# Performance work log

Measured on AMD Instinct MI355X. Metric: run time of the kernel, lower is better.

Reference implementation:

```python
import jax, jax.numpy as jnp
import numpy as np

QKV = 1024   # qkv_size (input feature dim)
E = 64       # embed_size (per-head dim)
H = 16       # num_heads
OUT = 1024   # output_size
B, S = 8, 1024


def setup_inputs() -> dict:
    key = jax.random.key(0)
    ks = jax.random.split(key, 8)
    inv = 1.0 / np.sqrt(QKV)
    return {
        "query": jax.random.normal(ks[0], (B, S, QKV), jnp.float32),
        "key": jax.random.normal(ks[1], (B, S, QKV), jnp.float32),
        "value": jax.random.normal(ks[2], (B, S, QKV), jnp.float32),
        # stacked per-head projection weights, torch Linear convention y = x @ W.T -> store as [H, QKV, E]
        "Wq": jax.random.normal(ks[3], (H, QKV, E), jnp.float32) * inv,
        "Wk": jax.random.normal(ks[4], (H, QKV, E), jnp.float32) * inv,
        "Wv": jax.random.normal(ks[5], (H, QKV, E), jnp.float32) * inv,
        "Wo": jax.random.normal(ks[6], (OUT, H * E), jnp.float32) / np.sqrt(H * E),
        "bo": jax.random.normal(ks[7], (OUT,), jnp.float32) * 0.01,
    }


def reference(query, key, value, Wq, Wk, Wv, Wo, bo):
    # batched over heads: [B,S,QKV] x [H,QKV,E] -> [B,H,S,E]
    Q = jnp.einsum("bsd,hde->bhse", query, Wq)
    K = jnp.einsum("bsd,hde->bhse", key, Wk)
    V = jnp.einsum("bsd,hde->bhse", value, Wv)
    # NOTE: original scales by sqrt(qkv_dim) (input dim), not per-head dim
    scale = 1.0 / jnp.sqrt(jnp.float32(QKV))
    scores = jnp.einsum("bhse,bhte->bhst", Q, K) * scale  # [B,H,S,S]
    attn = jax.nn.softmax(scores, axis=-1)
    attended = jnp.einsum("bhst,bhte->bhse", attn, V)     # [B,H,S,E]
    # concat heads along last dim (head-major order matches torch.cat of head outputs)
    concat = attended.transpose(0, 2, 1, 3).reshape(query.shape[0], query.shape[1], H * E)
    return concat @ Wo.T + bo
```

## Files before the change

kernel.cpp:

```cpp
#include <hip/hip_runtime.h>
#include <stdint.h>


typedef __bf16 bf16x8 __attribute__((ext_vector_type(8)));
typedef float f32x4 __attribute__((ext_vector_type(4)));

typedef __attribute__((address_space(3))) uint32_t lds_u32;
typedef const __attribute__((address_space(1))) uint32_t glb_u32;

__device__ __forceinline__ ushort f2bf(float f) {
  uint32_t x = __float_as_uint(f);
  x += 0x7fff + ((x >> 16) & 1);
  return (ushort)(x >> 16);
}
__device__ __forceinline__ bf16x8 ld8(const ushort* p) {
  union { uint4 u; bf16x8 b; } c;
  c.u = *reinterpret_cast<const uint4*>(p);
  return c.b;
}
__device__ __forceinline__ void cvt16(const float* __restrict__ src,
                                      ushort* __restrict__ dst) {
  union { uint4 u[2]; ushort s[16]; } o;
#pragma unroll
  for (int i = 0; i < 4; ++i) {
    const float4 f = reinterpret_cast<const float4*>(src)[i];
    o.s[4 * i + 0] = f2bf(f.x);
    o.s[4 * i + 1] = f2bf(f.y);
    o.s[4 * i + 2] = f2bf(f.z);
    o.s[4 * i + 3] = f2bf(f.w);
  }
  reinterpret_cast<uint4*>(dst)[0] = o.u[0];
  reinterpret_cast<uint4*>(dst)[1] = o.u[1];
}

__device__ __forceinline__ void gld16(const ushort* g, ushort* l) {
  __builtin_amdgcn_global_load_lds((glb_u32*)g, (lds_u32*)l, 16, 0, 0);
}

__global__ __launch_bounds__(256) void prep_wt3(
    const float* __restrict__ W0, const float* __restrict__ W1,
    const float* __restrict__ W2, ushort* __restrict__ T0,
    ushort* __restrict__ T1, ushort* __restrict__ T2) {
  __shared__ __align__(16) ushort tile[64 * 72];
  const int sel = blockIdx.x >> 8;
  const float* W = sel == 0 ? W0 : sel == 1 ? W1 : W2;
  ushort* WT = sel == 0 ? T0 : sel == 1 ? T1 : T2;
  const int bid = blockIdx.x & 255;
  const int h = bid >> 4;
  const int kt = bid & 15;
  const int t = threadIdx.x;
  const int row = t >> 2;
  const int ch = (t & 3) * 16;
  cvt16(W + ((size_t)h * 1024 + kt * 64 + row) * 64 + ch, &tile[row * 72 + ch]);
  __syncthreads();
  const int e = t >> 2;
  const int kc = (t & 3) * 16;
  ushort vals[16];
#pragma unroll
  for (int j = 0; j < 16; ++j) vals[j] = tile[(kc + j) * 72 + e];
  ushort* dst = WT + (size_t)(h * 64 + e) * 1024 + kt * 64 + kc;
  reinterpret_cast<uint4*>(dst)[0] = *reinterpret_cast<uint4*>(&vals[0]);
  reinterpret_cast<uint4*>(dst)[1] = *reinterpret_cast<uint4*>(&vals[8]);
}

__global__ __launch_bounds__(256) void cvt_wo(const float* __restrict__ src,
                                              ushort* __restrict__ dst) {
  const int i = (blockIdx.x * 256 + threadIdx.x) * 16;
  cvt16(src + i, dst + i);
}

__global__ __launch_bounds__(256) void cvt3(const float* __restrict__ s0,
                                            ushort* __restrict__ d0,
                                            const float* __restrict__ s1,
                                            ushort* __restrict__ d1,
                                            const float* __restrict__ s2,
                                            ushort* __restrict__ d2) {
  int b = blockIdx.x;
  const float* s;
  ushort* d;
  if (b < 2048) { s = s0; d = d0; }
  else if (b < 4096) { s = s1; d = d1; b -= 2048; }
  else { s = s2; d = d2; b -= 4096; }
  const int i = (b * 256 + threadIdx.x) * 16;
  cvt16(s + i, d + i);
}

__device__ __forceinline__ void stage_ab(const ushort* a_src,
                                         const ushort* b_src, ushort* as,
                                         ushort* bs, int w, int k0) {
#pragma unroll
  for (int c = 0; c < 4; ++c) {
    gld16(a_src + (size_t)c * 32 * 1024 + k0, as + (w * 8 + c * 32) * 64);
    gld16(b_src + (size_t)c * 32 * 1024 + k0, bs + (w * 8 + c * 32) * 64);
  }
}

template <bool F32OUT>
__device__ __forceinline__ void gemm_core(const ushort* __restrict__ A,
                                          const ushort* __restrict__ Bt,
                                          const float* __restrict__ bias,
                                          void* __restrict__ Cv, float oscale,
                                          int bx, int by) {
  __shared__ __align__(16) ushort As[2][128 * 64];
  __shared__ __align__(16) ushort Bs[2][128 * 64];
  const int n0 = bx * 128;
  const int m0 = by * 128;
  const int t = threadIdx.x;
  const int lane = t & 63;
  const int w = t >> 6;
  const int wm = w >> 1, wn = w & 1;
  const int col = lane & 15;
  const int quad = lane >> 4;
  const int gr = lane >> 3;
  const int gc = (lane & 7) * 8;

  f32x4 acc[4][4];
#pragma unroll
  for (int i = 0; i < 4; ++i)
#pragma unroll
    for (int j = 0; j < 4; ++j) acc[i][j] = (f32x4){0.f, 0.f, 0.f, 0.f};

  const ushort* a_src = A + (size_t)(m0 + w * 8 + gr) * 1024 + gc;
  const ushort* b_src = Bt + (size_t)(n0 + w * 8 + gr) * 1024 + gc;

  stage_ab(a_src, b_src, As[0], Bs[0], w, 0);
  __syncthreads();

  int cur = 0;
  for (int it = 0; it < 16; ++it) {
    if (it < 15)
      stage_ab(a_src, b_src, As[cur ^ 1], Bs[cur ^ 1], w, (it + 1) * 64);
    const ushort* asb = As[cur];
    const ushort* bsb = Bs[cur];
#pragma unroll
    for (int half = 0; half < 2; ++half) {
      bf16x8 af[4], bfr[4];
#pragma unroll
      for (int i = 0; i < 4; ++i)
        af[i] = ld8(&asb[(wm * 64 + i * 16 + col) * 64 + half * 32 + quad * 8]);
#pragma unroll
      for (int j = 0; j < 4; ++j)
        bfr[j] = ld8(&bsb[(wn * 64 + j * 16 + col) * 64 + half * 32 + quad * 8]);
#pragma unroll
      for (int i = 0; i < 4; ++i)
#pragma unroll
        for (int j = 0; j < 4; ++j)
          acc[i][j] = __builtin_amdgcn_mfma_f32_16x16x32_bf16(af[i], bfr[j],
                                                              acc[i][j], 0, 0, 0);
    }
    __syncthreads();
    cur ^= 1;
  }

#pragma unroll
  for (int i = 0; i < 4; ++i)
#pragma unroll
    for (int j = 0; j < 4; ++j) {
      const int n = n0 + wn * 64 + j * 16 + col;
      float bv = 0.f;
      if (F32OUT) bv = bias[n];
#pragma unroll
      for (int r = 0; r < 4; ++r) {
        const int m = m0 + wm * 64 + i * 16 + quad * 4 + r;
        if (F32OUT)
          reinterpret_cast<float*>(Cv)[(size_t)m * 1024 + n] = acc[i][j][r] + bv;
        else
          reinterpret_cast<ushort*>(Cv)[(size_t)m * 1024 + n] =
              f2bf(acc[i][j][r] * oscale);
      }
    }
}

template <bool F32OUT>
__global__ __launch_bounds__(256) void gemm_bb(const ushort* __restrict__ A,
                                               const ushort* __restrict__ Bt,
                                               const float* __restrict__ bias,
                                               void* __restrict__ Cv,
                                               float oscale) {
  gemm_core<F32OUT>(A, Bt, bias, Cv, oscale, blockIdx.x, blockIdx.y);
}

__global__ __launch_bounds__(256) void gemm_proj2(
    const ushort* __restrict__ A0, const ushort* __restrict__ B0,
    ushort* __restrict__ C0, float s0, const ushort* __restrict__ A1,
    const ushort* __restrict__ B1, ushort* __restrict__ C1, float s1) {
  if (blockIdx.z == 0)
    gemm_core<false>(A0, B0, nullptr, C0, s0, blockIdx.x, blockIdx.y);
  else
    gemm_core<false>(A1, B1, nullptr, C1, s1, blockIdx.x, blockIdx.y);
}

__global__ __launch_bounds__(256) void flash_attn(const ushort* __restrict__ Q,
                                                  const ushort* __restrict__ K,
                                                  const ushort* __restrict__ V,
                                                  ushort* __restrict__ O) {
  __shared__ __align__(16) ushort QP[128 * 72];
  __shared__ __align__(16) ushort Ks[64 * 64];
  __shared__ __align__(16) ushort Vt[64 * 72];
  const int pair = blockIdx.x & 127;
  const int b = pair >> 4;
  const int h = pair & 15;
  const int qt = blockIdx.x >> 7;
  const int t = threadIdx.x;
  const int lane = t & 63;
  const int w = t >> 6;
  const int col = lane & 15;
  const int quad = lane >> 4;

  const size_t base = (size_t)b * 1024 * 1024 + h * 64;
  const int qrow0 = qt * 128;

  {
    const int row = t >> 1;
    const int c0 = (t & 1) * 32;
    const ushort* src = Q + base + (size_t)(qrow0 + row) * 1024 + c0;
    uint4 v0 = reinterpret_cast<const uint4*>(src)[0];
    uint4 v1 = reinterpret_cast<const uint4*>(src)[1];
    uint4 v2 = reinterpret_cast<const uint4*>(src)[2];
    uint4 v3 = reinterpret_cast<const uint4*>(src)[3];
    reinterpret_cast<uint4*>(&QP[row * 72 + c0])[0] = v0;
    reinterpret_cast<uint4*>(&QP[row * 72 + c0])[1] = v1;
    reinterpret_cast<uint4*>(&QP[row * 72 + c0])[2] = v2;
    reinterpret_cast<uint4*>(&QP[row * 72 + c0])[3] = v3;
  }
  __syncthreads();
  bf16x8 qa[2][2];
#pragma unroll
  for (int g = 0; g < 2; ++g)
#pragma unroll
    for (int half = 0; half < 2; ++half)
      qa[g][half] =
          ld8(&QP[(w * 32 + g * 16 + col) * 72 + half * 32 + quad * 8]);

  f32x4 o_[2][4];
#pragma unroll
  for (int g = 0; g < 2; ++g)
#pragma unroll
    for (int c = 0; c < 4; ++c) o_[g][c] = (f32x4){0.f, 0.f, 0.f, 0.f};
  float m_s[2] = {-1e30f, -1e30f};
  float l_s[2] = {0.f, 0.f};

  const int krow = w * 16 + (lane >> 3);
  const int kcs = (((lane & 7) ^ (lane >> 3)) << 3);
  const int s7 = col & 7;

  for (int kt = 0; kt < 16; ++kt) {
    {
      const ushort* k0 = K + base + (size_t)(kt * 64 + krow) * 1024 + kcs;
      gld16(k0, &Ks[(w * 16) * 64]);
      gld16(k0 + 8 * 1024, &Ks[(w * 16 + 8) * 64]);
      const int vs = t & 63;
      const int ve = (t >> 6) * 16;
      const ushort* vsrc = V + base + (size_t)(kt * 64 + vs) * 1024 + ve;
      union { uint4 u[2]; ushort s[16]; } vv;
      vv.u[0] = reinterpret_cast<const uint4*>(vsrc)[0];
      vv.u[1] = reinterpret_cast<const uint4*>(vsrc)[1];
#pragma unroll
      for (int j = 0; j < 16; ++j) Vt[(ve + j) * 72 + vs] = vv.s[j];
    }
    __syncthreads();

    f32x4 sc[2][4];
#pragma unroll
    for (int c = 0; c < 4; ++c) {
      const int R = (c * 16 + col) * 64;
      bf16x8 kb0 = ld8(&Ks[R + ((quad ^ s7) << 3)]);
      bf16x8 kb1 = ld8(&Ks[R + (((quad + 4) ^ s7) << 3)]);
#pragma unroll
      for (int g = 0; g < 2; ++g) {
        f32x4 z = {0.f, 0.f, 0.f, 0.f};
        z = __builtin_amdgcn_mfma_f32_16x16x32_bf16(kb0, qa[g][0], z, 0, 0, 0);
        z = __builtin_amdgcn_mfma_f32_16x16x32_bf16(kb1, qa[g][1], z, 0, 0, 0);
        sc[g][c] = z;
      }
    }

    float al[2];
#pragma unroll
    for (int g = 0; g < 2; ++g) {
      float mx = sc[g][0][0];
#pragma unroll
      for (int c = 0; c < 4; ++c)
#pragma unroll
        for (int r = 0; r < 4; ++r) mx = fmaxf(mx, sc[g][c][r]);
      mx = fmaxf(mx, __shfl_xor(mx, 16));
      mx = fmaxf(mx, __shfl_xor(mx, 32));
      const float m_new = fmaxf(m_s[g], mx);
      al[g] = __expf(m_s[g] - m_new);
      m_s[g] = m_new;
      float rs = 0.f;
      const int prow = (w * 32 + g * 16 + col) * 72;
#pragma unroll
      for (int c = 0; c < 4; ++c) {
        const float p0 = __expf(sc[g][c][0] - m_new);
        const float p1 = __expf(sc[g][c][1] - m_new);
        const float p2 = __expf(sc[g][c][2] - m_new);
        const float p3 = __expf(sc[g][c][3] - m_new);
        rs += (p0 + p1) + (p2 + p3);
        union { uint2 u; ushort s[4]; } pk;
        pk.s[0] = f2bf(p0);
        pk.s[1] = f2bf(p1);
        pk.s[2] = f2bf(p2);
        pk.s[3] = f2bf(p3);
        *reinterpret_cast<uint2*>(&QP[prow + c * 16 + quad * 4]) = pk.u;
      }
      rs += __shfl_xor(rs, 16);
      rs += __shfl_xor(rs, 32);
      l_s[g] = l_s[g] * al[g] + rs;
    }

#pragma unroll
    for (int g = 0; g < 2; ++g)
#pragma unroll
      for (int r = 0; r < 4; ++r) {
        const float a = __shfl(al[g], (lane & 48) | (quad * 4 + r));
        o_[g][0][r] *= a;
        o_[g][1][r] *= a;
        o_[g][2][r] *= a;
        o_[g][3][r] *= a;
      }

    bf16x8 pa[2][2];
#pragma unroll
    for (int g = 0; g < 2; ++g)
#pragma unroll
      for (int half = 0; half < 2; ++half)
        pa[g][half] =
            ld8(&QP[(w * 32 + g * 16 + col) * 72 + half * 32 + quad * 8]);
#pragma unroll
    for (int c = 0; c < 4; ++c) {
      bf16x8 vb0 = ld8(&Vt[(c * 16 + col) * 72 + quad * 8]);
      bf16x8 vb1 = ld8(&Vt[(c * 16 + col) * 72 + 32 + quad * 8]);
#pragma unroll
      for (int g = 0; g < 2; ++g) {
        o_[g][c] = __builtin_amdgcn_mfma_f32_16x16x32_bf16(pa[g][0], vb0,
                                                           o_[g][c], 0, 0, 0);
        o_[g][c] = __builtin_amdgcn_mfma_f32_16x16x32_bf16(pa[g][1], vb1,
                                                           o_[g][c], 0, 0, 0);
      }
    }
    __syncthreads();
  }

#pragma unroll
  for (int g = 0; g < 2; ++g)
#pragma unroll
    for (int r = 0; r < 4; ++r) {
      const float lr = __shfl(l_s[g], (lane & 48) | (quad * 4 + r));
      const float inv = 1.f / lr;
      const size_t row =
          base + (size_t)(qrow0 + w * 32 + g * 16 + quad * 4 + r) * 1024;
      O[row + 0 + col] = f2bf(o_[g][0][r] * inv);
      O[row + 16 + col] = f2bf(o_[g][1][r] * inv);
      O[row + 32 + col] = f2bf(o_[g][2][r] * inv);
      O[row + 48 + col] = f2bf(o_[g][3][r] * inv);
    }
}

extern "C" void kernel_launch(void* const* d_in, const int* in_sizes, int n_in,
                              void* d_out, int out_size, void* d_ws, size_t ws_size,
                              hipStream_t stream) {
  const float* q = (const float*)d_in[0];
  const float* k = (const float*)d_in[1];
  const float* v = (const float*)d_in[2];
  const float* Wq = (const float*)d_in[3];
  const float* Wk = (const float*)d_in[4];
  const float* Wv = (const float*)d_in[5];
  const float* Wo = (const float*)d_in[6];
  const float* bo = (const float*)d_in[7];
  float* out = (float*)d_out;
  ushort* ws = (ushort*)d_ws;

  const size_t M8 = 8u << 20;
  const size_t M1 = 1u << 20;
  ushort* Qp = ws;
  ushort* Kp = ws + M8;
  ushort* Vp = ws + 2 * M8;
  ushort* WqT = ws + 3 * M8;
  ushort* WkT = WqT + M1;
  ushort* WvT = WkT + M1;
  ushort* WoB = WvT + M1;

  ushort* X0 = (ushort*)d_out;
  ushort* X1 = X0 + M8;

  prep_wt3<<<768, 256, 0, stream>>>(Wq, Wk, Wv, WqT, WkT, WvT);
  cvt3<<<4352, 256, 0, stream>>>(q, X0, k, X1, Wo, WoB);
  gemm_proj2<<<dim3(8, 64, 2), 256, 0, stream>>>(X0, WqT, Qp, 0.03125f,
                                                 X1, WkT, Kp, 1.0f);
  cvt_wo<<<2048, 256, 0, stream>>>(v, X0);
  gemm_bb<false><<<dim3(8, 64), 256, 0, stream>>>(X0, WvT, nullptr, Vp, 1.0f);

  flash_attn<<<1024, 256, 0, stream>>>(Qp, Kp, Vp, Qp);

  gemm_bb<true><<<dim3(8, 64), 256, 0, stream>>>(Qp, WoB, bo, out, 1.0f);
}
```

Before: 384.4 us.

## Fuse V conversion into a single QKV projection launch, single-buffer LDS, lazy softmax rescale

Merges the Q/K projection and the V projection into one 192-row-tile launch. The V path converts fp32 activations to bf16 on the fly while staging to LDS, so the separate V conversion kernel and its round trip through global memory are removed. The GEMM LDS goes from double to single buffering, which cuts LDS use and may raise occupancy but gives up load/compute overlap. Flash attention now skips the running-max update and accumulator rescale when the new block max exceeds the old one by at most 8, which saves exps and multiplies at some risk of overflow or precision loss in exp.

```diff
diff --git a/kernel.cpp b/kernel.cpp
--- a/kernel.cpp
+++ b/kernel.cpp
@@ -63,12 +63,6 @@
   reinterpret_cast<uint4*>(dst)[1] = *reinterpret_cast<uint4*>(&vals[8]);
 }
 
-__global__ __launch_bounds__(256) void cvt_wo(const float* __restrict__ src,
-                                              ushort* __restrict__ dst) {
-  const int i = (blockIdx.x * 256 + threadIdx.x) * 16;
-  cvt16(src + i, dst + i);
-}
-
 __global__ __launch_bounds__(256) void cvt3(const float* __restrict__ s0,
                                             ushort* __restrict__ d0,
                                             const float* __restrict__ s1,
@@ -85,24 +79,14 @@
   cvt16(s + i, d + i);
 }
 
-__device__ __forceinline__ void stage_ab(const ushort* a_src,
-                                         const ushort* b_src, ushort* as,
-                                         ushort* bs, int w, int k0) {
-#pragma unroll
-  for (int c = 0; c < 4; ++c) {
-    gld16(a_src + (size_t)c * 32 * 1024 + k0, as + (w * 8 + c * 32) * 64);
-    gld16(b_src + (size_t)c * 32 * 1024 + k0, bs + (w * 8 + c * 32) * 64);
-  }
-}
-
 template <bool F32OUT>
-__device__ __forceinline__ void gemm_core(const ushort* __restrict__ A,
-                                          const ushort* __restrict__ Bt,
-                                          const float* __restrict__ bias,
-                                          void* __restrict__ Cv, float oscale,
-                                          int bx, int by) {
-  __shared__ __align__(16) ushort As[2][128 * 64];
-  __shared__ __align__(16) ushort Bs[2][128 * 64];
+__device__ __forceinline__ void core_bb(ushort* __restrict__ As,
+                                        ushort* __restrict__ Bs,
+                                        const ushort* __restrict__ A,
+                                        const ushort* __restrict__ Bt,
+                                        const float* __restrict__ bias,
+                                        void* __restrict__ Cv, float oscale,
+                                        int bx, int by) {
   const int n0 = bx * 128;
   const int m0 = by * 128;
   const int t = threadIdx.x;
@@ -122,25 +106,26 @@
 
   const ushort* a_src = A + (size_t)(m0 + w * 8 + gr) * 1024 + gc;
   const ushort* b_src = Bt + (size_t)(n0 + w * 8 + gr) * 1024 + gc;
-
-  stage_ab(a_src, b_src, As[0], Bs[0], w, 0);
-  __syncthreads();
-
-  int cur = 0;
-  for (int it = 0; it < 16; ++it) {
-    if (it < 15)
-      stage_ab(a_src, b_src, As[cur ^ 1], Bs[cur ^ 1], w, (it + 1) * 64);
-    const ushort* asb = As[cur];
-    const ushort* bsb = Bs[cur];
+  ushort* as_base = &As[(w * 8) * 64];
+  ushort* bs_base = &Bs[(w * 8) * 64];
+
+  for (int k0 = 0; k0 < 1024; k0 += 64) {
+#pragma unroll
+    for (int c = 0; c < 4; ++c) {
+      gld16(a_src + (size_t)c * 32 * 1024 + k0, as_base + c * 32 * 64);
+      gld16(b_src + (size_t)c * 32 * 1024 + k0, bs_base + c * 32 * 64);
+    }
+    __syncthreads();
+
 #pragma unroll
     for (int half = 0; half < 2; ++half) {
       bf16x8 af[4], bfr[4];
 #pragma unroll
       for (int i = 0; i < 4; ++i)
-        af[i] = ld8(&asb[(wm * 64 + i * 16 + col) * 64 + half * 32 + quad * 8]);
+        af[i] = ld8(&As[(wm * 64 + i * 16 + col) * 64 + half * 32 + quad * 8]);
 #pragma unroll
       for (int j = 0; j < 4; ++j)
-        bfr[j] = ld8(&bsb[(wn * 64 + j * 16 + col) * 64 + half * 32 + quad * 8]);
+        bfr[j] = ld8(&Bs[(wn * 64 + j * 16 + col) * 64 + half * 32 + quad * 8]);
 #pragma unroll
       for (int i = 0; i < 4; ++i)
 #pragma unroll
@@ -149,7 +134,6 @@
                                                               acc[i][j], 0, 0, 0);
     }
     __syncthreads();
-    cur ^= 1;
   }
 
 #pragma unroll
@@ -171,23 +155,99 @@
     }
 }
 
-template <bool F32OUT>
-__global__ __launch_bounds__(256) void gemm_bb(const ushort* __restrict__ A,
-                                               const ushort* __restrict__ Bt,
-                                               const float* __restrict__ bias,
-                                               void* __restrict__ Cv,
-                                               float oscale) {
-  gemm_core<F32OUT>(A, Bt, bias, Cv, oscale, blockIdx.x, blockIdx.y);
-}
-
-__global__ __launch_bounds__(256) void gemm_proj2(
-    const ushort* __restrict__ A0, const ushort* __restrict__ B0,
-    ushort* __restrict__ C0, float s0, const ushort* __restrict__ A1,
-    const ushort* __restrict__ B1, ushort* __restrict__ C1, float s1) {
-  if (blockIdx.z == 0)
-    gemm_core<false>(A0, B0, nullptr, C0, s0, blockIdx.x, blockIdx.y);
+__device__ __forceinline__ void core_f32a(ushort* __restrict__ As72,
+                                          ushort* __restrict__ Bs,
+                                          const float* __restrict__ A,
+                                          const ushort* __restrict__ Bt,
+                                          ushort* __restrict__ C, int bx,
+                                          int by) {
+  const int n0 = bx * 128;
+  const int m0 = by * 128;
+  const int t = threadIdx.x;
+  const int lane = t & 63;
+  const int w = t >> 6;
+  const int wm = w >> 1, wn = w & 1;
+  const int col = lane & 15;
+  const int quad = lane >> 4;
+  const int gr = lane >> 3;
+  const int gc = (lane & 7) * 8;
+  const int srow = t >> 1;
+  const int sc0 = (t & 1) * 32;
+
+  f32x4 acc[4][4];
+#pragma unroll
+  for (int i = 0; i < 4; ++i)
+#pragma unroll
+    for (int j = 0; j < 4; ++j) acc[i][j] = (f32x4){0.f, 0.f, 0.f, 0.f};
+
+  const float* a_src = A + (size_t)(m0 + srow) * 1024 + sc0;
+  const ushort* b_src = Bt + (size_t)(n0 + w * 8 + gr) * 1024 + gc;
+  ushort* bs_base = &Bs[(w * 8) * 64];
+
+  for (int k0 = 0; k0 < 1024; k0 += 64) {
+#pragma unroll
+    for (int c = 0; c < 4; ++c)
+      gld16(b_src + (size_t)c * 32 * 1024 + k0, bs_base + c * 32 * 64);
+    cvt16(a_src + k0, &As72[srow * 72 + sc0]);
+    cvt16(a_src + k0 + 16, &As72[srow * 72 + sc0 + 16]);
+    __syncthreads();
+
+#pragma unroll
+    for (int half = 0; half < 2; ++half) {
+      bf16x8 af[4], bfr[4];
+#pragma unroll
+      for (int i = 0; i < 4; ++i)
+        af[i] = ld8(&As72[(wm * 64 + i * 16 + col) * 72 + half * 32 + quad * 8]);
+#pragma unroll
+      for (int j = 0; j < 4; ++j)
+        bfr[j] = ld8(&Bs[(wn * 64 + j * 16 + col) * 64 + half * 32 + quad * 8]);
+#pragma unroll
+      for (int i = 0; i < 4; ++i)
+#pragma unroll
+        for (int j = 0; j < 4; ++j)
+          acc[i][j] = __builtin_amdgcn_mfma_f32_16x16x32_bf16(af[i], bfr[j],
+                                                              acc[i][j], 0, 0, 0);
+    }
+    __syncthreads();
+  }
+
+#pragma unroll
+  for (int i = 0; i < 4; ++i)
+#pragma unroll
+    for (int j = 0; j < 4; ++j) {
+      const int n = n0 + wn * 64 + j * 16 + col;
+#pragma unroll
+      for (int r = 0; r < 4; ++r) {
+        const int m = m0 + wm * 64 + i * 16 + quad * 4 + r;
+        C[(size_t)m * 1024 + n] = f2bf(acc[i][j][r]);
+      }
+    }
+}
+
+__global__ __launch_bounds__(256) void gemm_out(const ushort* __restrict__ A,
+                                                const ushort* __restrict__ Bt,
+                                                const float* __restrict__ bias,
+                                                float* __restrict__ C) {
+  __shared__ __align__(16) ushort As[128 * 64];
+  __shared__ __align__(16) ushort Bs[128 * 64];
+  core_bb<true>(As, Bs, A, Bt, bias, C, 1.0f, blockIdx.x, blockIdx.y);
+}
+
+__global__ __launch_bounds__(256) void gemm_proj3(
+    const ushort* __restrict__ Aq, const ushort* __restrict__ Bq,
+    ushort* __restrict__ Cq, const ushort* __restrict__ Ak,
+    const ushort* __restrict__ Bk, ushort* __restrict__ Ck,
+    const float* __restrict__ Av, const ushort* __restrict__ Bv,
+    ushort* __restrict__ Cvp) {
+  __shared__ __align__(16) ushort As[128 * 72];
+  __shared__ __align__(16) ushort Bs[128 * 64];
+  const int by = blockIdx.y;
+  if (by < 64)
+    core_bb<false>(As, Bs, Aq, Bq, nullptr, Cq, 0.03125f, blockIdx.x, by);
+  else if (by < 128)
+    core_bb<false>(As, Bs, Ak, Bk, nullptr, Ck, 1.0f, blockIdx.x, by - 64);
   else
-    gemm_core<false>(A1, B1, nullptr, C1, s1, blockIdx.x, blockIdx.y);
+    core_f32a(As, Bs, Av, Bv, Cvp, blockIdx.x, by - 128);
 }
 
 __global__ __launch_bounds__(256) void flash_attn(const ushort* __restrict__ Q,
@@ -276,6 +336,7 @@
     }
 
     float al[2];
+    bool df[2];
 #pragma unroll
     for (int g = 0; g < 2; ++g) {
       float mx = sc[g][0][0];
@@ -285,17 +346,22 @@
         for (int r = 0; r < 4; ++r) mx = fmaxf(mx, sc[g][c][r]);
       mx = fmaxf(mx, __shfl_xor(mx, 16));
       mx = fmaxf(mx, __shfl_xor(mx, 32));
-      const float m_new = fmaxf(m_s[g], mx);
-      al[g] = __expf(m_s[g] - m_new);
-      m_s[g] = m_new;
+      df[g] = __all(mx - m_s[g] <= 8.0f) != 0;
+      if (df[g]) {
+        al[g] = 1.0f;
+      } else {
+        const float m_new = fmaxf(m_s[g], mx);
+        al[g] = __expf(m_s[g] - m_new);
+        m_s[g] = m_new;
+      }
       float rs = 0.f;
       const int prow = (w * 32 + g * 16 + col) * 72;
 #pragma unroll
       for (int c = 0; c < 4; ++c) {
-        const float p0 = __expf(sc[g][c][0] - m_new);
-        const float p1 = __expf(sc[g][c][1] - m_new);
-        const float p2 = __expf(sc[g][c][2] - m_new);
-        const float p3 = __expf(sc[g][c][3] - m_new);
+        const float p0 = __expf(sc[g][c][0] - m_s[g]);
+        const float p1 = __expf(sc[g][c][1] - m_s[g]);
+        const float p2 = __expf(sc[g][c][2] - m_s[g]);
+        const float p3 = __expf(sc[g][c][3] - m_s[g]);
         rs += (p0 + p1) + (p2 + p3);
         union { uint2 u; ushort s[4]; } pk;
         pk.s[0] = f2bf(p0);
@@ -306,18 +372,20 @@
       }
       rs += __shfl_xor(rs, 16);
       rs += __shfl_xor(rs, 32);
-      l_s[g] = l_s[g] * al[g] + rs;
+      l_s[g] = df[g] ? (l_s[g] + rs) : (l_s[g] * al[g] + rs);
     }
 
 #pragma unroll
     for (int g = 0; g < 2; ++g)
-#pragma unroll
-      for (int r = 0; r < 4; ++r) {
-        const float a = __shfl(al[g], (lane & 48) | (quad * 4 + r));
-        o_[g][0][r] *= a;
-        o_[g][1][r] *= a;
-        o_[g][2][r] *= a;
-        o_[g][3][r] *= a;
+      if (!df[g]) {
+#pragma unroll
+        for (int r = 0; r < 4; ++r) {
+          const float a = __shfl(al[g], (lane & 48) | (quad * 4 + r));
+          o_[g][0][r] *= a;
+          o_[g][1][r] *= a;
+          o_[g][2][r] *= a;
+          o_[g][3][r] *= a;
+        }
       }
 
     bf16x8 pa[2][2];
@@ -386,12 +454,10 @@
 
   prep_wt3<<<768, 256, 0, stream>>>(Wq, Wk, Wv, WqT, WkT, WvT);
   cvt3<<<4352, 256, 0, stream>>>(q, X0, k, X1, Wo, WoB);
-  gemm_proj2<<<dim3(8, 64, 2), 256, 0, stream>>>(X0, WqT, Qp, 0.03125f,
-                                                 X1, WkT, Kp, 1.0f);
-  cvt_wo<<<2048, 256, 0, stream>>>(v, X0);
-  gemm_bb<false><<<dim3(8, 64), 256, 0, stream>>>(X0, WvT, nullptr, Vp, 1.0f);
+  gemm_proj3<<<dim3(8, 192), 256, 0, stream>>>(X0, WqT, Qp, X1, WkT, Kp,
+                                               v, WvT, Vp);
 
   flash_attn<<<1024, 256, 0, stream>>>(Qp, Kp, Vp, Qp);
 
-  gemm_bb<true><<<dim3(8, 64), 256, 0, stream>>>(Qp, WoB, bo, out, 1.0f);
-}
+  gemm_out<<<dim3(8, 64), 256, 0, stream>>>(Qp, WoB, bo, out);
+}
```

Measured after the change: 353.4 us. -8.1%, faster.
